# Kernel tuning notes

Measured on AMD Instinct MI355X. Metric: run time of the kernel, lower is better.

The kernel has to match this reference:

```python
import jax, jax.numpy as jnp
import numpy as np

NUM_HEADS = 16
INPUT_DIM = 1024  # == dim == qkv_scale


def setup_inputs() -> dict:
    key = jax.random.key(0)
    k1, k2, k3 = jax.random.split(key, 3)
    x = jax.random.normal(k1, (4, 2048, INPUT_DIM), dtype=jnp.float32)
    # torch Linear(input_dim, 3*dim): y = x @ W.T + b; we store W pre-transposed as [in, out]
    W_qkv = jax.random.normal(k2, (INPUT_DIM, 3 * INPUT_DIM), dtype=jnp.float32) * (INPUT_DIM ** -0.5)
    b_qkv = jax.random.normal(k3, (3 * INPUT_DIM,), dtype=jnp.float32) * 0.01
    return {"x": x, "W_qkv": W_qkv, "b_qkv": b_qkv}


def reference(x, W_qkv, b_qkv):
    b, n, _ = x.shape
    h = NUM_HEADS
    d = INPUT_DIM // h
    scale = INPUT_DIM ** 0.5  # qkv_scale**0.5, MULTIPLIED (no softmax, no division)

    qkv = x @ W_qkv + b_qkv                      # [b, n, 3*dim]
    # rearrange 'b n (h d k) -> k b h n d': last axis splits (h, d, 3), k fastest
    qkv = qkv.reshape(b, n, h, d, 3)
    q = jnp.transpose(qkv[..., 0], (0, 2, 1, 3))  # [b, h, n, d]
    k_ = jnp.transpose(qkv[..., 1], (0, 2, 1, 3))
    v = jnp.transpose(qkv[..., 2], (0, 2, 1, 3))

    attn = jnp.einsum('bhid,bhjd->bhij', q, k_) * scale  # [b, h, n, n]
    out = jnp.einsum('bhij,bhjd->bhid', attn, v)         # [b, h, n, d]
    return out
```

## Files before the change

### kernel.cpp

```cpp
#include <hip/hip_runtime.h>
#include <stdint.h>

#define DEV __device__ __forceinline__

typedef float f32x4 __attribute__((ext_vector_type(4)));
typedef __bf16 bf16x8 __attribute__((ext_vector_type(8)));
typedef short short8 __attribute__((ext_vector_type(8)));
typedef short short4v __attribute__((ext_vector_type(4)));

DEV unsigned short f2bf(float f) {
    union { float f; unsigned u; } c; c.f = f;
    unsigned u = c.u;
    u += 0x7fffu + ((u >> 16) & 1u);
    return (unsigned short)(u >> 16);
}

DEV void async_ld16(const void* g, void* l) {
    __builtin_amdgcn_global_load_lds(
        (const __attribute__((address_space(1))) unsigned int*)g,
        (__attribute__((address_space(3))) unsigned int*)l, 16, 0, 0);
}

DEV f32x4 mfma16(bf16x8 a, bf16x8 b, f32x4 c) {
    return __builtin_amdgcn_mfma_f32_16x16x32_bf16(a, b, c, 0, 0, 0);
}

__global__ __launch_bounds__(256) void k_cvt_x(const float* __restrict__ x,
                                               unsigned short* __restrict__ xb) {
    int t = blockIdx.x * 256 + threadIdx.x;
    const float4* xp = (const float4*)x;
    float4 a = xp[t * 2], b = xp[t * 2 + 1];
    short8 o;
    o[0] = (short)f2bf(a.x); o[1] = (short)f2bf(a.y);
    o[2] = (short)f2bf(a.z); o[3] = (short)f2bf(a.w);
    o[4] = (short)f2bf(b.x); o[5] = (short)f2bf(b.y);
    o[6] = (short)f2bf(b.z); o[7] = (short)f2bf(b.w);
    *(short8*)(xb + t * 8) = o;
}

__global__ __launch_bounds__(256) void k_tr_w(const float* __restrict__ W,
                                              unsigned short* __restrict__ Wt) {
    __shared__ float T[64][65];
    int n0 = blockIdx.x * 64, k0 = blockIdx.y * 64;
    int t = threadIdx.x;
    int r = t >> 4, c4 = (t & 15) * 4;
    for (int i = 0; i < 4; i++) {
        int row = r + i * 16;
        float4 v = *(const float4*)(W + (k0 + row) * 3072 + n0 + c4);
        T[row][c4] = v.x; T[row][c4 + 1] = v.y; T[row][c4 + 2] = v.z; T[row][c4 + 3] = v.w;
    }
    __syncthreads();
    for (int i = 0; i < 4; i++) {
        int nrow = r + i * 16;
        short4v o;
        o[0] = (short)f2bf(T[c4 + 0][nrow]);
        o[1] = (short)f2bf(T[c4 + 1][nrow]);
        o[2] = (short)f2bf(T[c4 + 2][nrow]);
        o[3] = (short)f2bf(T[c4 + 3][nrow]);
        *(short4v*)(Wt + (n0 + nrow) * 1024 + k0 + c4) = o;
    }
}

__global__ __launch_bounds__(256, 2) void k_qkv(const unsigned short* __restrict__ xb,
                                                const unsigned short* __restrict__ Wt,
                                                const float* __restrict__ bias,
                                                unsigned short* __restrict__ Q,
                                                unsigned short* __restrict__ K,
                                                unsigned short* __restrict__ V) {
    __shared__ __align__(16) unsigned short As[128 * 64];
    __shared__ __align__(16) unsigned short Bs[128 * 64];
    const int m0 = blockIdx.y * 128, n0 = blockIdx.x * 128;
    const int wave = threadIdx.x >> 6, lane = threadIdx.x & 63;
    const int wm = (wave & 1) * 64, wn = (wave >> 1) * 64;
    f32x4 acc[4][4] = {};
    const int slr = wave * 32 + (lane >> 3);
    const int scs = lane & 7;

    for (int kt = 0; kt < 16; kt++) {
        __syncthreads();
        for (int i = 0; i < 4; i++) {
            int lr = slr + i * 8;
            int c = scs ^ (lr & 7);
            async_ld16(xb + (m0 + lr) * 1024 + kt * 64 + c * 8,
                       (void*)(As + (wave * 32 + i * 8) * 64));
            async_ld16(Wt + (n0 + lr) * 1024 + kt * 64 + c * 8,
                       (void*)(Bs + (wave * 32 + i * 8) * 64));
        }
        __syncthreads();
        for (int ks = 0; ks < 2; ks++) {
            bf16x8 af[4], bfr[4];
            int c0 = ks * 4 + (lane >> 4);
            for (int tm = 0; tm < 4; tm++) {
                int row = wm + tm * 16 + (lane & 15);
                af[tm] = *(const bf16x8*)(As + row * 64 + (c0 ^ (row & 7)) * 8);
            }
            for (int tn = 0; tn < 4; tn++) {
                int row = wn + tn * 16 + (lane & 15);
                bfr[tn] = *(const bf16x8*)(Bs + row * 64 + (c0 ^ (row & 7)) * 8);
            }
            for (int tm = 0; tm < 4; tm++)
                for (int tn = 0; tn < 4; tn++)
                    acc[tm][tn] = mfma16(af[tm], bfr[tn], acc[tm][tn]);
        }
    }

    const int batch = m0 >> 11;
    for (int tn = 0; tn < 4; tn++) {
        int col = n0 + wn + tn * 16 + (lane & 15);
        int h = col / 192;
        int rem = col - h * 192;
        int d = rem / 3;
        int which = rem - d * 3;
        float bv = bias[col];
        int bh = batch * 16 + h;
        unsigned q_base = (unsigned)bh * 131072u + (unsigned)d;
        unsigned kv_base = ((unsigned)bh * 64u + (unsigned)d) * 2048u;
        unsigned short* dst = which == 0 ? Q : (which == 1 ? K : V);
        float mult = which == 0 ? 32.0f : 1.0f;
        for (int tm = 0; tm < 4; tm++) {
            int rbase = m0 + wm + tm * 16 + ((lane >> 4) * 4);
            for (int r = 0; r < 4; r++) {
                int row = rbase + r;
                unsigned token = (unsigned)(row & 2047);
                float val = (acc[tm][tn][r] + bv) * mult;
                unsigned idx = (which == 0) ? (q_base + token * 64u) : (kv_base + token);
                dst[idx] = f2bf(val);
            }
        }
    }
}

__global__ __launch_bounds__(256) void k_kv(const unsigned short* __restrict__ Kt,
                                            const unsigned short* __restrict__ Vt,
                                            float* __restrict__ Mpart) {
    __shared__ __align__(16) float Ss[3][4096];
    const int bh = blockIdx.y, ns = blockIdx.x;
    const int wave = threadIdx.x >> 6, lane = threadIdx.x & 63;
    const int lan15 = lane & 15, quad = lane >> 4;
    const unsigned base = (unsigned)bh * 131072u;
    const int n0w = ns * 512 + wave * 128;
    f32x4 acc[4][4] = {};
#pragma unroll
    for (int ks = 0; ks < 4; ks++) {
        bf16x8 af[4], bfr[4];
        int no = n0w + ks * 32 + quad * 8;
        for (int mt = 0; mt < 4; mt++)
            af[mt] = *(const bf16x8*)(Kt + base + (unsigned)(mt * 16 + lan15) * 2048u + no);
        for (int nt = 0; nt < 4; nt++)
            bfr[nt] = *(const bf16x8*)(Vt + base + (unsigned)(nt * 16 + lan15) * 2048u + no);
        for (int mt = 0; mt < 4; mt++)
            for (int nt = 0; nt < 4; nt++)
                acc[mt][nt] = mfma16(af[mt], bfr[nt], acc[mt][nt]);
    }
    if (wave >= 1) {
        for (int mt = 0; mt < 4; mt++)
            for (int nt = 0; nt < 4; nt++)
                *(f32x4*)(&Ss[wave - 1][((mt * 4 + nt) * 64 + lane) * 4]) = acc[mt][nt];
    }
    __syncthreads();
    if (wave == 0) {
        float* dst = Mpart + ((unsigned)bh * 4u + (unsigned)ns) * 4096u;
        for (int mt = 0; mt < 4; mt++)
            for (int nt = 0; nt < 4; nt++) {
                f32x4 o = acc[mt][nt];
                for (int s = 0; s < 3; s++) {
                    f32x4 p = *(const f32x4*)(&Ss[s][((mt * 4 + nt) * 64 + lane) * 4]);
                    o.x += p.x; o.y += p.y; o.z += p.z; o.w += p.w;
                }
                *(f32x4*)(dst + ((mt * 4 + nt) * 64 + lane) * 4) = o;
            }
    }
}

__global__ __launch_bounds__(256, 2) void k_qm(const unsigned short* __restrict__ Q,
                                               const float* __restrict__ Mpart,
                                               float* __restrict__ out) {
    __shared__ __align__(16) unsigned short Msb[64 * 64];
    const int bh = blockIdx.y;
    const int q0 = blockIdx.x * 256;
    const int t = threadIdx.x;
    const int wave = t >> 6, lane = t & 63;
    const int lan15 = lane & 15, quad = lane >> 4;
    const unsigned base = (unsigned)bh * 131072u;

    {
        const float* mp = Mpart + (unsigned)bh * 4u * 4096u;
        int e0 = t * 16;
        for (int j = 0; j < 4; j++) {
            f32x4 m = *(const f32x4*)(mp + e0 + j * 4);
            for (int s = 1; s < 4; s++) {
                f32x4 p = *(const f32x4*)(mp + s * 4096 + e0 + j * 4);
                m.x += p.x; m.y += p.y; m.z += p.z; m.w += p.w;
            }
            for (int r = 0; r < 4; r++) {
                int e = e0 + j * 4 + r;
                int tile = e >> 8, le = (e >> 2) & 63;
                int d1 = (tile >> 2) * 16 + ((le >> 4) << 2) + r;
                int d2 = (tile & 3) * 16 + (le & 15);
                Msb[d2 * 64 + (((d1 >> 3) ^ (d2 & 7)) << 3) + (d1 & 7)] = f2bf(m[r]);
            }
        }
    }
    __syncthreads();

    const int q0w = q0 + wave * 64;
    f32x4 oacc[4][4] = {};
#pragma unroll
    for (int ks = 0; ks < 2; ks++) {
        bf16x8 af[4], bfr[4];
        for (int mt = 0; mt < 4; mt++)
            af[mt] = *(const bf16x8*)(Q + base + (unsigned)(q0w + mt * 16 + lan15) * 64u +
                                      ks * 32 + quad * 8);
        for (int nt = 0; nt < 4; nt++) {
            int d2 = nt * 16 + lan15;
            bfr[nt] = *(const bf16x8*)(Msb + d2 * 64 + (((ks * 4 + quad) ^ (d2 & 7)) << 3));
        }
        for (int mt = 0; mt < 4; mt++)
            for (int nt = 0; nt < 4; nt++)
                oacc[mt][nt] = mfma16(af[mt], bfr[nt], oacc[mt][nt]);
    }
    for (int mt = 0; mt < 4; mt++)
        for (int nt = 0; nt < 4; nt++)
            for (int r = 0; r < 4; r++)
                out[base + (unsigned)(q0w + mt * 16 + quad * 4 + r) * 64u + nt * 16 + lan15] =
                    oacc[mt][nt][r];
}

extern "C" void kernel_launch(void* const* d_in, const int* in_sizes, int n_in,
                              void* d_out, int out_size, void* d_ws, size_t ws_size,
                              hipStream_t stream) {
    const float* x = (const float*)d_in[0];
    const float* W = (const float*)d_in[1];
    const float* b = (const float*)d_in[2];
    float* out = (float*)d_out;

    unsigned short* xb = (unsigned short*)d_ws;
    unsigned short* Wt = xb + 8388608;
    unsigned short* Qb = Wt + 3145728;
    unsigned short* Kt = Qb + 8388608;
    unsigned short* Vt = Kt + 8388608;
    float* Mpart = (float*)d_ws;

    k_cvt_x<<<4096, 256, 0, stream>>>(x, xb);
    k_tr_w<<<dim3(48, 16), 256, 0, stream>>>(W, Wt);
    k_qkv<<<dim3(24, 64), 256, 0, stream>>>(xb, Wt, b, Qb, Kt, Vt);
    k_kv<<<dim3(4, 64), 256, 0, stream>>>(Kt, Vt, Mpart);
    k_qm<<<dim3(8, 64), 256, 0, stream>>>(Qb, Mpart, out);
}
```

Before: 200.6 us.

## Merge prep kernels and fuse KV and QM stages with atomic counter barrier

Combines the x conversion and W transpose into one launch that also zeroes per-head counters, and fuses the K^T V reduction with the Q·M product into one kernel. Blocks for the same head synchronise through an atomic counter spin-wait rather than a separate launch, and the KV reduction is split over 8 partial slices instead of 4. This removes two kernel launches and their gaps. It relies on all 512 blocks being co-resident to avoid deadlock, and adds spin-wait and partial-sum traffic.

```diff
diff --git a/kernel.cpp b/kernel.cpp
--- a/kernel.cpp
+++ b/kernel.cpp
@@ -25,39 +25,45 @@
     return __builtin_amdgcn_mfma_f32_16x16x32_bf16(a, b, c, 0, 0, 0);
 }
 
-__global__ __launch_bounds__(256) void k_cvt_x(const float* __restrict__ x,
-                                               unsigned short* __restrict__ xb) {
-    int t = blockIdx.x * 256 + threadIdx.x;
-    const float4* xp = (const float4*)x;
-    float4 a = xp[t * 2], b = xp[t * 2 + 1];
-    short8 o;
-    o[0] = (short)f2bf(a.x); o[1] = (short)f2bf(a.y);
-    o[2] = (short)f2bf(a.z); o[3] = (short)f2bf(a.w);
-    o[4] = (short)f2bf(b.x); o[5] = (short)f2bf(b.y);
-    o[6] = (short)f2bf(b.z); o[7] = (short)f2bf(b.w);
-    *(short8*)(xb + t * 8) = o;
-}
-
-__global__ __launch_bounds__(256) void k_tr_w(const float* __restrict__ W,
-                                              unsigned short* __restrict__ Wt) {
+__global__ __launch_bounds__(256) void k_prep(const float* __restrict__ x,
+                                              const float* __restrict__ W,
+                                              unsigned short* __restrict__ xb,
+                                              unsigned short* __restrict__ Wt,
+                                              unsigned int* __restrict__ ctr) {
     __shared__ float T[64][65];
-    int n0 = blockIdx.x * 64, k0 = blockIdx.y * 64;
-    int t = threadIdx.x;
-    int r = t >> 4, c4 = (t & 15) * 4;
-    for (int i = 0; i < 4; i++) {
-        int row = r + i * 16;
-        float4 v = *(const float4*)(W + (k0 + row) * 3072 + n0 + c4);
-        T[row][c4] = v.x; T[row][c4 + 1] = v.y; T[row][c4 + 2] = v.z; T[row][c4 + 3] = v.w;
-    }
-    __syncthreads();
-    for (int i = 0; i < 4; i++) {
-        int nrow = r + i * 16;
-        short4v o;
-        o[0] = (short)f2bf(T[c4 + 0][nrow]);
-        o[1] = (short)f2bf(T[c4 + 1][nrow]);
-        o[2] = (short)f2bf(T[c4 + 2][nrow]);
-        o[3] = (short)f2bf(T[c4 + 3][nrow]);
-        *(short4v*)(Wt + (n0 + nrow) * 1024 + k0 + c4) = o;
+    int blk = blockIdx.x;
+    if (blk < 4096) {
+        int t = blk * 256 + threadIdx.x;
+        const float4* xp = (const float4*)x;
+        float4 a = xp[t * 2], b = xp[t * 2 + 1];
+        short8 o;
+        o[0] = (short)f2bf(a.x); o[1] = (short)f2bf(a.y);
+        o[2] = (short)f2bf(a.z); o[3] = (short)f2bf(a.w);
+        o[4] = (short)f2bf(b.x); o[5] = (short)f2bf(b.y);
+        o[6] = (short)f2bf(b.z); o[7] = (short)f2bf(b.w);
+        *(short8*)(xb + t * 8) = o;
+    } else if (blk < 4864) {
+        int bx = blk - 4096;
+        int n0 = (bx % 48) * 64, k0 = (bx / 48) * 64;
+        int t = threadIdx.x;
+        int r = t >> 4, c4 = (t & 15) * 4;
+        for (int i = 0; i < 4; i++) {
+            int row = r + i * 16;
+            float4 v = *(const float4*)(W + (k0 + row) * 3072 + n0 + c4);
+            T[row][c4] = v.x; T[row][c4 + 1] = v.y; T[row][c4 + 2] = v.z; T[row][c4 + 3] = v.w;
+        }
+        __syncthreads();
+        for (int i = 0; i < 4; i++) {
+            int nrow = r + i * 16;
+            short4v o;
+            o[0] = (short)f2bf(T[c4 + 0][nrow]);
+            o[1] = (short)f2bf(T[c4 + 1][nrow]);
+            o[2] = (short)f2bf(T[c4 + 2][nrow]);
+            o[3] = (short)f2bf(T[c4 + 3][nrow]);
+            *(short4v*)(Wt + (n0 + nrow) * 1024 + k0 + c4) = o;
+        }
+    } else {
+        if (threadIdx.x < 128) ctr[threadIdx.x] = 0u;
     }
 }
 
@@ -130,65 +136,70 @@
     }
 }
 
-__global__ __launch_bounds__(256) void k_kv(const unsigned short* __restrict__ Kt,
-                                            const unsigned short* __restrict__ Vt,
-                                            float* __restrict__ Mpart) {
+__global__ __launch_bounds__(256) void k_attn2(const unsigned short* __restrict__ Kt,
+                                               const unsigned short* __restrict__ Vt,
+                                               const unsigned short* __restrict__ Q,
+                                               float* __restrict__ Mpart,
+                                               unsigned int* __restrict__ ctr,
+                                               float* __restrict__ out) {
     __shared__ __align__(16) float Ss[3][4096];
-    const int bh = blockIdx.y, ns = blockIdx.x;
+    const int i = blockIdx.x;
+    const int bh = i >> 3, sub = i & 7;
     const int wave = threadIdx.x >> 6, lane = threadIdx.x & 63;
     const int lan15 = lane & 15, quad = lane >> 4;
     const unsigned base = (unsigned)bh * 131072u;
-    const int n0w = ns * 512 + wave * 128;
-    f32x4 acc[4][4] = {};
+
+    {
+        const int n0w = sub * 256 + wave * 64;
+        f32x4 acc[4][4] = {};
 #pragma unroll
-    for (int ks = 0; ks < 4; ks++) {
-        bf16x8 af[4], bfr[4];
-        int no = n0w + ks * 32 + quad * 8;
-        for (int mt = 0; mt < 4; mt++)
-            af[mt] = *(const bf16x8*)(Kt + base + (unsigned)(mt * 16 + lan15) * 2048u + no);
-        for (int nt = 0; nt < 4; nt++)
-            bfr[nt] = *(const bf16x8*)(Vt + base + (unsigned)(nt * 16 + lan15) * 2048u + no);
-        for (int mt = 0; mt < 4; mt++)
+        for (int ks = 0; ks < 2; ks++) {
+            bf16x8 af[4], bfr[4];
+            int no = n0w + ks * 32 + quad * 8;
+            for (int mt = 0; mt < 4; mt++)
+                af[mt] = *(const bf16x8*)(Kt + base + (unsigned)(mt * 16 + lan15) * 2048u + no);
             for (int nt = 0; nt < 4; nt++)
-                acc[mt][nt] = mfma16(af[mt], bfr[nt], acc[mt][nt]);
-    }
-    if (wave >= 1) {
-        for (int mt = 0; mt < 4; mt++)
-            for (int nt = 0; nt < 4; nt++)
-                *(f32x4*)(&Ss[wave - 1][((mt * 4 + nt) * 64 + lane) * 4]) = acc[mt][nt];
+                bfr[nt] = *(const bf16x8*)(Vt + base + (unsigned)(nt * 16 + lan15) * 2048u + no);
+            for (int mt = 0; mt < 4; mt++)
+                for (int nt = 0; nt < 4; nt++)
+                    acc[mt][nt] = mfma16(af[mt], bfr[nt], acc[mt][nt]);
+        }
+        if (wave >= 1) {
+            for (int mt = 0; mt < 4; mt++)
+                for (int nt = 0; nt < 4; nt++)
+                    *(f32x4*)(&Ss[wave - 1][((mt * 4 + nt) * 64 + lane) * 4]) = acc[mt][nt];
+        }
+        __syncthreads();
+        if (wave == 0) {
+            float* dst = Mpart + ((unsigned)bh * 8u + (unsigned)sub) * 4096u;
+            for (int mt = 0; mt < 4; mt++)
+                for (int nt = 0; nt < 4; nt++) {
+                    f32x4 o = acc[mt][nt];
+                    for (int s = 0; s < 3; s++) {
+                        f32x4 p = *(const f32x4*)(&Ss[s][((mt * 4 + nt) * 64 + lane) * 4]);
+                        o.x += p.x; o.y += p.y; o.z += p.z; o.w += p.w;
+                    }
+                    *(f32x4*)(dst + ((mt * 4 + nt) * 64 + lane) * 4) = o;
+                }
+            __threadfence();
+            if (lane == 0)
+                __hip_atomic_fetch_add(&ctr[bh], 1u, __ATOMIC_RELEASE, __HIP_MEMORY_SCOPE_AGENT);
+        }
+    }
+
+    if (threadIdx.x == 0) {
+        while (__hip_atomic_load(&ctr[bh], __ATOMIC_ACQUIRE, __HIP_MEMORY_SCOPE_AGENT) < 8u)
+            __builtin_amdgcn_s_sleep(8);
     }
     __syncthreads();
-    if (wave == 0) {
-        float* dst = Mpart + ((unsigned)bh * 4u + (unsigned)ns) * 4096u;
-        for (int mt = 0; mt < 4; mt++)
-            for (int nt = 0; nt < 4; nt++) {
-                f32x4 o = acc[mt][nt];
-                for (int s = 0; s < 3; s++) {
-                    f32x4 p = *(const f32x4*)(&Ss[s][((mt * 4 + nt) * 64 + lane) * 4]);
-                    o.x += p.x; o.y += p.y; o.z += p.z; o.w += p.w;
-                }
-                *(f32x4*)(dst + ((mt * 4 + nt) * 64 + lane) * 4) = o;
-            }
-    }
-}
-
-__global__ __launch_bounds__(256, 2) void k_qm(const unsigned short* __restrict__ Q,
-                                               const float* __restrict__ Mpart,
-                                               float* __restrict__ out) {
-    __shared__ __align__(16) unsigned short Msb[64 * 64];
-    const int bh = blockIdx.y;
-    const int q0 = blockIdx.x * 256;
-    const int t = threadIdx.x;
-    const int wave = t >> 6, lane = t & 63;
-    const int lan15 = lane & 15, quad = lane >> 4;
-    const unsigned base = (unsigned)bh * 131072u;
-
+
+    unsigned short* Msb = (unsigned short*)&Ss[0][0];
     {
-        const float* mp = Mpart + (unsigned)bh * 4u * 4096u;
-        int e0 = t * 16;
+        const float* mp = Mpart + (unsigned)bh * 8u * 4096u;
+        int e0 = threadIdx.x * 16;
         for (int j = 0; j < 4; j++) {
             f32x4 m = *(const f32x4*)(mp + e0 + j * 4);
-            for (int s = 1; s < 4; s++) {
+            for (int s = 1; s < 8; s++) {
                 f32x4 p = *(const f32x4*)(mp + s * 4096 + e0 + j * 4);
                 m.x += p.x; m.y += p.y; m.z += p.z; m.w += p.w;
             }
@@ -203,27 +214,29 @@
     }
     __syncthreads();
 
-    const int q0w = q0 + wave * 64;
-    f32x4 oacc[4][4] = {};
+    {
+        const int q0w = sub * 256 + wave * 64;
+        f32x4 oacc[4][4] = {};
 #pragma unroll
-    for (int ks = 0; ks < 2; ks++) {
-        bf16x8 af[4], bfr[4];
-        for (int mt = 0; mt < 4; mt++)
-            af[mt] = *(const bf16x8*)(Q + base + (unsigned)(q0w + mt * 16 + lan15) * 64u +
-                                      ks * 32 + quad * 8);
-        for (int nt = 0; nt < 4; nt++) {
-            int d2 = nt * 16 + lan15;
-            bfr[nt] = *(const bf16x8*)(Msb + d2 * 64 + (((ks * 4 + quad) ^ (d2 & 7)) << 3));
+        for (int ks = 0; ks < 2; ks++) {
+            bf16x8 af[4], bfr[4];
+            for (int mt = 0; mt < 4; mt++)
+                af[mt] = *(const bf16x8*)(Q + base + (unsigned)(q0w + mt * 16 + lan15) * 64u +
+                                          ks * 32 + quad * 8);
+            for (int nt = 0; nt < 4; nt++) {
+                int d2 = nt * 16 + lan15;
+                bfr[nt] = *(const bf16x8*)(Msb + d2 * 64 + (((ks * 4 + quad) ^ (d2 & 7)) << 3));
+            }
+            for (int mt = 0; mt < 4; mt++)
+                for (int nt = 0; nt < 4; nt++)
+                    oacc[mt][nt] = mfma16(af[mt], bfr[nt], oacc[mt][nt]);
         }
         for (int mt = 0; mt < 4; mt++)
             for (int nt = 0; nt < 4; nt++)
-                oacc[mt][nt] = mfma16(af[mt], bfr[nt], oacc[mt][nt]);
-    }
-    for (int mt = 0; mt < 4; mt++)
-        for (int nt = 0; nt < 4; nt++)
-            for (int r = 0; r < 4; r++)
-                out[base + (unsigned)(q0w + mt * 16 + quad * 4 + r) * 64u + nt * 16 + lan15] =
-                    oacc[mt][nt][r];
+                for (int r = 0; r < 4; r++)
+                    out[base + (unsigned)(q0w + mt * 16 + quad * 4 + r) * 64u + nt * 16 + lan15] =
+                        oacc[mt][nt][r];
+    }
 }
 
 extern "C" void kernel_launch(void* const* d_in, const int* in_sizes, int n_in,
@@ -239,11 +252,10 @@
     unsigned short* Qb = Wt + 3145728;
     unsigned short* Kt = Qb + 8388608;
     unsigned short* Vt = Kt + 8388608;
+    unsigned int* ctr = (unsigned int*)(Vt + 8388608);
     float* Mpart = (float*)d_ws;
 
-    k_cvt_x<<<4096, 256, 0, stream>>>(x, xb);
-    k_tr_w<<<dim3(48, 16), 256, 0, stream>>>(W, Wt);
+    k_prep<<<4865, 256, 0, stream>>>(x, W, xb, Wt, ctr);
     k_qkv<<<dim3(24, 64), 256, 0, stream>>>(xb, Wt, b, Qb, Kt, Vt);
-    k_kv<<<dim3(4, 64), 256, 0, stream>>>(Kt, Vt, Mpart);
-    k_qm<<<dim3(8, 64), 256, 0, stream>>>(Qb, Mpart, out);
-}
+    k_attn2<<<512, 256, 0, stream>>>(Kt, Vt, Qb, Mpart, ctr, out);
+}
```

Result: slower. 243.2 us (+21.2%).
